# Optimization experiments

Measured on AMD Instinct MI355X. Metric: run time of the kernel, lower is better.

## Reference

```python
import jax, jax.numpy as jnp
import numpy as np

N, L, D, H, R = 16384, 8, 256, 256, 64  # nodes, chain len, input dim, hidden dim, rel dim


def setup_inputs() -> dict:
    key = jax.random.key(0)
    ks = jax.random.split(key, 10)
    s = 1.0 / np.sqrt(H)
    f32 = jnp.float32
    return {
        "left_chain": jax.random.normal(ks[0], (N, L, D), f32),
        "right_chain": jax.random.normal(ks[1], (N, L, D), f32),
        "rel": jax.random.normal(ks[2], (N, R), f32),
        "Wih_l": jax.random.normal(ks[3], (4 * H, D), f32) * s,
        "Whh_l": jax.random.normal(ks[4], (4 * H, H), f32) * s,
        "bih_l": jnp.zeros((4 * H,), f32),
        "bhh_l": jnp.zeros((4 * H,), f32),
        "Wih_r": jax.random.normal(ks[5], (4 * H, D), f32) * s,
        "Whh_r": jax.random.normal(ks[6], (4 * H, H), f32) * s,
        "bih_r": jnp.zeros((4 * H,), f32),
        "bhh_r": jnp.zeros((4 * H,), f32),
        "Wenc": jax.random.normal(ks[7], (H, 2 * H + R), f32) * s,
        "benc": jnp.zeros((H,), f32),
    }


def _lstm_last(x, Wih, Whh, bih, bhh):
    # x: [N, L, D]; PyTorch LSTM gate order i, f, g, o; zero initial state.
    n = x.shape[0]
    h0 = jnp.zeros((n, Whh.shape[1]), x.dtype)
    b = bih + bhh

    def step(carry, xt):
        h, c = carry
        g = xt @ Wih.T + h @ Whh.T + b  # [N, 4H]
        i, f, gg, o = jnp.split(g, 4, axis=-1)
        c = jax.nn.sigmoid(f) * c + jax.nn.sigmoid(i) * jnp.tanh(gg)
        h = jax.nn.sigmoid(o) * jnp.tanh(c)
        return (h, c), None

    (h, _c), _ = jax.lax.scan(step, (h0, h0), jnp.swapaxes(x, 0, 1))
    return h  # final hidden state [N, H]


def reference(left_chain, right_chain, rel,
              Wih_l, Whh_l, bih_l, bhh_l,
              Wih_r, Whh_r, bih_r, bhh_r,
              Wenc, benc):
    hl = _lstm_last(left_chain, Wih_l, Whh_l, bih_l, bhh_l)   # el(t)
    hr = _lstm_last(right_chain, Wih_r, Whh_r, bih_r, bhh_r)  # er(t)
    con = jnp.concatenate([hl, hr, rel], axis=-1)             # [N, 2H+R]
    return jnp.tanh(con @ Wenc.T + benc)                      # enc(t): [N, H]
```

## Files before the change

kernel.cpp:

```cpp
#include <hip/hip_runtime.h>
#include <hip/hip_fp16.h>

#define N_NODES 16384
#define SEQ_L   8
#define DIM_D   256
#define DIM_H   256
#define DIM_R   64

typedef float    f32x4 __attribute__((ext_vector_type(4)));
typedef _Float16 f16x8 __attribute__((ext_vector_type(8)));
typedef _Float16 f16x4 __attribute__((ext_vector_type(4)));

__device__ __forceinline__ float fsig(float x) {
    return __builtin_amdgcn_rcpf(1.f + __expf(-x));
}
__device__ __forceinline__ float ftanh(float x) {
    return 1.f - 2.f * __builtin_amdgcn_rcpf(1.f + __expf(2.f * x));
}

__global__ void prep_kernel(const float* __restrict__ Wih_l, const float* __restrict__ Whh_l,
                            const float* __restrict__ Wih_r, const float* __restrict__ Whh_r,
                            const float* __restrict__ Wenc,  const float* __restrict__ rel,
                            _Float16* __restrict__ pih_l, _Float16* __restrict__ phh_l,
                            _Float16* __restrict__ pih_r, _Float16* __restrict__ phh_r,
                            _Float16* __restrict__ penc,  _Float16* __restrict__ rel16) {
    const int stride = gridDim.x * blockDim.x;
    const int t0 = blockIdx.x * blockDim.x + threadIdx.x;

    const float* SW[4] = {Wih_l, Whh_l, Wih_r, Whh_r};
    _Float16*    DW[4] = {pih_l, phh_l, pih_r, phh_r};
    for (int m = 0; m < 4; ++m) {
        const float* W = SW[m];
        _Float16*    P = DW[m];
        for (int i8 = t0; i8 < 32768; i8 += stride) {
            int w    = i8 >> 12;
            int rem  = i8 & 4095;
            int f    = rem >> 6;
            int lane = rem & 63;
            int g    = f >> 4;
            int ht   = (f >> 3) & 1;
            int ks   = f & 7;
            int col  = g * 256 + w * 32 + ht * 16 + (lane & 15);
            int k    = ks * 32 + (lane >> 4) * 8;
            const float* s = W + (size_t)col * 256 + k;
            f32x4 v0 = *(const f32x4*)s;
            f32x4 v1 = *(const f32x4*)(s + 4);
            f16x8 h;
            h[0] = (_Float16)v0[0]; h[1] = (_Float16)v0[1];
            h[2] = (_Float16)v0[2]; h[3] = (_Float16)v0[3];
            h[4] = (_Float16)v1[0]; h[5] = (_Float16)v1[1];
            h[6] = (_Float16)v1[2]; h[7] = (_Float16)v1[3];
            *(f16x8*)&P[(size_t)i8 * 8] = h;
        }
    }

    for (int i8 = t0; i8 < 18432; i8 += stride) {
        int w    = i8 / 4608;
        int rem  = i8 - w * 4608;
        int f    = rem >> 6;
        int lane = rem & 63;
        int ct   = f / 18;
        int ks   = f - ct * 18;
        int col  = w * 64 + ct * 16 + (lane & 15);
        int k    = ks * 32 + (lane >> 4) * 8;
        const float* s = Wenc + (size_t)col * 576 + k;
        f32x4 v0 = *(const f32x4*)s;
        f32x4 v1 = *(const f32x4*)(s + 4);
        f16x8 h;
        h[0] = (_Float16)v0[0]; h[1] = (_Float16)v0[1];
        h[2] = (_Float16)v0[2]; h[3] = (_Float16)v0[3];
        h[4] = (_Float16)v1[0]; h[5] = (_Float16)v1[1];
        h[6] = (_Float16)v1[2]; h[7] = (_Float16)v1[3];
        *(f16x8*)&penc[(size_t)i8 * 8] = h;
    }

    const int nq = (N_NODES * DIM_R) / 8;
    for (int i = t0; i < nq; i += stride) {
        f32x4 v0 = *(const f32x4*)(rel + (size_t)i * 8);
        f32x4 v1 = *(const f32x4*)(rel + (size_t)i * 8 + 4);
        f16x8 h;
        h[0] = (_Float16)v0[0]; h[1] = (_Float16)v0[1];
        h[2] = (_Float16)v0[2]; h[3] = (_Float16)v0[3];
        h[4] = (_Float16)v1[0]; h[5] = (_Float16)v1[1];
        h[6] = (_Float16)v1[2]; h[7] = (_Float16)v1[3];
        *(f16x8*)&rel16[(size_t)i * 8] = h;
    }
}

__global__ __launch_bounds__(512, 2) void lstm_kernel(
    const float* __restrict__ left, const float* __restrict__ right,
    const _Float16* __restrict__ pih_l, const _Float16* __restrict__ phh_l,
    const _Float16* __restrict__ pih_r, const _Float16* __restrict__ phh_r,
    const float* __restrict__ bih_l, const float* __restrict__ bhh_l,
    const float* __restrict__ bih_r, const float* __restrict__ bhh_r,
    _Float16* __restrict__ hl_out, _Float16* __restrict__ hr_out) {

    const int side = blockIdx.y;
    const float*    chain = side ? right : left;
    const float*    bih   = side ? bih_r : bih_l;
    const float*    bhh   = side ? bhh_r : bhh_l;
    _Float16*       hout  = side ? hr_out : hl_out;

    __shared__ _Float16 lds[2 * 64 * 256] __attribute__((aligned(16)));

    const int tid  = threadIdx.x;
    const int lane = tid & 63;
    const int wave = tid >> 6;
    const int wu   = __builtin_amdgcn_readfirstlane(wave);
    const int l15  = lane & 15;
    const int l4   = lane >> 4;
    const int klb  = l4 * 8;
    const int node0 = blockIdx.x * 64;
    const int hid0  = wu * 32;

    const _Float16* Pih = (side ? pih_r : pih_l) + wu * 32768;
    const _Float16* Phh = (side ? phh_r : phh_l) + wu * 32768;

    const f32x4 FZ = {0.f, 0.f, 0.f, 0.f};

    float bias[4][2];
#pragma unroll
    for (int g = 0; g < 4; ++g)
#pragma unroll
        for (int ht = 0; ht < 2; ++ht) {
            int col = g * 256 + hid0 + ht * 16 + l15;
            bias[g][ht] = bih[col] + bhh[col];
        }

    f32x4 acc[4][4][2];
    f32x4 cst[4][2];
#pragma unroll
    for (int rt = 0; rt < 4; ++rt)
#pragma unroll
        for (int ht = 0; ht < 2; ++ht) cst[rt][ht] = FZ;

    int abase[4];
#pragma unroll
    for (int rt = 0; rt < 4; ++rt) {
        int row = rt * 16 + l15;
        abase[rt] = row * 256 + (klb ^ ((row & 3) << 3));
    }

    auto do_gemm = [&](const int lds_ofs, const _Float16* Pw) {
#pragma unroll
        for (int ks = 0; ks < 8; ++ks) {
            f16x8 a[4];
#pragma unroll
            for (int rt = 0; rt < 4; ++rt)
                a[rt] = *(const f16x8*)&lds[lds_ofs + abase[rt] + ks * 32];
            f16x8 b[8];
#pragma unroll
            for (int f = 0; f < 8; ++f)
                b[f] = *(const f16x8*)&Pw[(f * 8 + ks) * 512 + (lane << 3)];
#pragma unroll
            for (int g = 0; g < 4; ++g)
#pragma unroll
                for (int ht = 0; ht < 2; ++ht)
#pragma unroll
                    for (int rt = 0; rt < 4; ++rt)
                        acc[rt][g][ht] = __builtin_amdgcn_mfma_f32_16x16x32_f16(
                            a[rt], b[g * 2 + ht], acc[rt][g][ht], 0, 0, 0);
        }
    };

#pragma unroll 1
    for (int t = 0; t < SEQ_L; ++t) {
#pragma unroll
        for (int it = 0; it < 8; ++it) {
            int e4  = it * 512 + tid;
            int row = e4 >> 6;
            int kq  = (e4 & 63) << 2;
            f32x4 v = __builtin_nontemporal_load((const f32x4*)(chain +
                      (size_t)(node0 + row) * (SEQ_L * DIM_D) + t * DIM_D + kq));
            f16x4 h4;
            h4[0] = (_Float16)v[0]; h4[1] = (_Float16)v[1];
            h4[2] = (_Float16)v[2]; h4[3] = (_Float16)v[3];
            *(f16x4*)&lds[row * 256 + (kq ^ ((row & 3) << 3))] = h4;
        }
        __syncthreads();

#pragma unroll
        for (int rt = 0; rt < 4; ++rt)
#pragma unroll
            for (int g = 0; g < 4; ++g)
#pragma unroll
                for (int ht = 0; ht < 2; ++ht) acc[rt][g][ht] = FZ;

        do_gemm(0, Pih);
        if (t > 0) do_gemm(16384, Phh);
        __syncthreads();

#pragma unroll
        for (int rt = 0; rt < 4; ++rt)
#pragma unroll
            for (int ht = 0; ht < 2; ++ht)
#pragma unroll
                for (int r = 0; r < 4; ++r) {
                    float gi = acc[rt][0][ht][r] + bias[0][ht];
                    float gf = acc[rt][1][ht][r] + bias[1][ht];
                    float gg = acc[rt][2][ht][r] + bias[2][ht];
                    float go = acc[rt][3][ht][r] + bias[3][ht];
                    float ii = fsig(gi), ff = fsig(gf);
                    float gt = ftanh(gg), oo = fsig(go);
                    float c = ff * cst[rt][ht][r] + ii * gt;
                    cst[rt][ht][r] = c;
                    float h = oo * ftanh(c);
                    int rowl = rt * 16 + l4 * 4 + r;
                    int hid  = hid0 + ht * 16 + l15;
                    lds[16384 + rowl * 256 + (hid ^ ((rowl & 3) << 3))] = (_Float16)h;
                }
    }

    __syncthreads();
    {
        int row = tid >> 3;
        int seg = (tid & 7) * 32;
        _Float16* dst = hout + (size_t)(node0 + row) * 256 + seg;
        int sw = (row & 3) << 3;
#pragma unroll
        for (int j = 0; j < 4; ++j) {
            f16x8 v = *(const f16x8*)&lds[16384 + row * 256 + ((seg + j * 8) ^ sw)];
            __builtin_nontemporal_store(v, (f16x8*)(dst + j * 8));
        }
    }
}

__global__ __launch_bounds__(256, 2) void enc_kernel(
    const _Float16* __restrict__ hl, const _Float16* __restrict__ hr,
    const _Float16* __restrict__ rel16, const _Float16* __restrict__ penc,
    const float* __restrict__ benc, float* __restrict__ out) {

    const int tid  = threadIdx.x;
    const int lane = tid & 63;
    const int wave = tid >> 6;
    const int wu   = __builtin_amdgcn_readfirstlane(wave);
    const int l15  = lane & 15;
    const int l4   = lane >> 4;
    const int klb  = l4 * 8;
    const int row0 = blockIdx.x * 64;
    const int colw = wu * 64;

    const _Float16* Pw = penc + wu * 36864;

    const f32x4 FZ = {0.f, 0.f, 0.f, 0.f};
    f32x4 acc[4][4];
#pragma unroll
    for (int rt = 0; rt < 4; ++rt)
#pragma unroll
        for (int ct = 0; ct < 4; ++ct) acc[rt][ct] = FZ;

    float bce[4];
#pragma unroll
    for (int ct = 0; ct < 4; ++ct) bce[ct] = benc[colw + ct * 16 + l15];

    for (int ks = 0; ks < 18; ++ks) {
        const int kk = ks * 32 + klb;
        f16x8 a[4];
#pragma unroll
        for (int rt = 0; rt < 4; ++rt) {
            int row = row0 + rt * 16 + l15;
            const _Float16* p;
            if (ks < 8)       p = hl    + (size_t)row * 256 + kk;
            else if (ks < 16) p = hr    + (size_t)row * 256 + (kk - 256);
            else              p = rel16 + (size_t)row * 64  + (kk - 512);
            a[rt] = *(const f16x8*)p;
        }
#pragma unroll
        for (int ct = 0; ct < 4; ++ct) {
            f16x8 b = *(const f16x8*)&Pw[(ct * 18 + ks) * 512 + (lane << 3)];
#pragma unroll
            for (int rt = 0; rt < 4; ++rt)
                acc[rt][ct] = __builtin_amdgcn_mfma_f32_16x16x32_f16(
                    a[rt], b, acc[rt][ct], 0, 0, 0);
        }
    }

#pragma unroll
    for (int rt = 0; rt < 4; ++rt)
#pragma unroll
        for (int ct = 0; ct < 4; ++ct)
#pragma unroll
            for (int r = 0; r < 4; ++r) {
                int row = row0 + rt * 16 + l4 * 4 + r;
                int col = colw + ct * 16 + l15;
                out[(size_t)row * 256 + col] = ftanh(acc[rt][ct][r] + bce[ct]);
            }
}

extern "C" void kernel_launch(void* const* d_in, const int* in_sizes, int n_in,
                              void* d_out, int out_size, void* d_ws, size_t ws_size,
                              hipStream_t stream) {
    const float* left  = (const float*)d_in[0];
    const float* right = (const float*)d_in[1];
    const float* rel   = (const float*)d_in[2];
    const float* Wih_l = (const float*)d_in[3];
    const float* Whh_l = (const float*)d_in[4];
    const float* bih_l = (const float*)d_in[5];
    const float* bhh_l = (const float*)d_in[6];
    const float* Wih_r = (const float*)d_in[7];
    const float* Whh_r = (const float*)d_in[8];
    const float* bih_r = (const float*)d_in[9];
    const float* bhh_r = (const float*)d_in[10];
    const float* Wenc  = (const float*)d_in[11];
    const float* benc  = (const float*)d_in[12];
    float* out = (float*)d_out;

    char* ws = (char*)d_ws;
    _Float16* pih_l = (_Float16*)(ws);
    _Float16* phh_l = (_Float16*)(ws + 512 * 1024);
    _Float16* pih_r = (_Float16*)(ws + 1024 * 1024);
    _Float16* phh_r = (_Float16*)(ws + 1536 * 1024);
    _Float16* penc  = (_Float16*)(ws + 2048 * 1024);
    _Float16* rel16 = (_Float16*)(ws + 2560 * 1024);
    _Float16* hl16  = (_Float16*)(ws + 4608 * 1024);
    _Float16* hr16  = (_Float16*)(ws + 4608 * 1024 + 8192 * 1024);
    (void)in_sizes; (void)n_in; (void)out_size; (void)ws_size;

    hipLaunchKernelGGL(prep_kernel, dim3(512), dim3(256), 0, stream,
                       Wih_l, Whh_l, Wih_r, Whh_r, Wenc, rel,
                       pih_l, phh_l, pih_r, phh_r, penc, rel16);

    hipLaunchKernelGGL(lstm_kernel, dim3(N_NODES / 64, 2), dim3(512), 0, stream,
                       left, right, pih_l, phh_l, pih_r, phh_r,
                       bih_l, bhh_l, bih_r, bhh_r, hl16, hr16);

    hipLaunchKernelGGL(enc_kernel, dim3(N_NODES / 64), dim3(256), 0, stream,
                       hl16, hr16, rel16, penc, benc, out);
}
```

Before: 1.401 ms.

## Shrink LSTM tile to 32 nodes with 16 waves of 16 hidden units each

The LSTM kernel is retiled from 64 nodes × 8 waves (32 hidden units per wave) to 32 nodes × 16 waves (16 hidden units per wave). The weight prepacking layout changes to match. This cuts accumulator registers and LDS per block, which allows more blocks per CU and better latency hiding. In exchange, each weight fragment loaded from global/L2 is reused across only two row tiles instead of four, so weight traffic per node doubles.

```diff
diff --git a/kernel.cpp b/kernel.cpp
--- a/kernel.cpp
+++ b/kernel.cpp
@@ -33,14 +33,13 @@
         const float* W = SW[m];
         _Float16*    P = DW[m];
         for (int i8 = t0; i8 < 32768; i8 += stride) {
-            int w    = i8 >> 12;
-            int rem  = i8 & 4095;
+            int w    = i8 >> 11;
+            int rem  = i8 & 2047;
             int f    = rem >> 6;
             int lane = rem & 63;
-            int g    = f >> 4;
-            int ht   = (f >> 3) & 1;
-            int ks   = f & 7;
-            int col  = g * 256 + w * 32 + ht * 16 + (lane & 15);
+            int ks   = f >> 2;
+            int g    = f & 3;
+            int col  = g * 256 + w * 16 + (lane & 15);
             int k    = ks * 32 + (lane >> 4) * 8;
             const float* s = W + (size_t)col * 256 + k;
             f32x4 v0 = *(const f32x4*)s;
@@ -87,7 +86,7 @@
     }
 }
 
-__global__ __launch_bounds__(512, 2) void lstm_kernel(
+__global__ __launch_bounds__(1024, 4) void lstm_kernel(
     const float* __restrict__ left, const float* __restrict__ right,
     const _Float16* __restrict__ pih_l, const _Float16* __restrict__ phh_l,
     const _Float16* __restrict__ pih_r, const _Float16* __restrict__ phh_r,
@@ -101,7 +100,8 @@
     const float*    bhh   = side ? bhh_r : bhh_l;
     _Float16*       hout  = side ? hr_out : hl_out;
 
-    __shared__ _Float16 lds[2 * 64 * 256] __attribute__((aligned(16)));
+    __shared__ _Float16 lds[2 * 32 * 256] __attribute__((aligned(16)));
+    const int HOFF = 32 * 256;
 
     const int tid  = threadIdx.x;
     const int lane = tid & 63;
@@ -110,33 +110,28 @@
     const int l15  = lane & 15;
     const int l4   = lane >> 4;
     const int klb  = l4 * 8;
-    const int node0 = blockIdx.x * 64;
-    const int hid0  = wu * 32;
-
-    const _Float16* Pih = (side ? pih_r : pih_l) + wu * 32768;
-    const _Float16* Phh = (side ? phh_r : phh_l) + wu * 32768;
+    const int node0 = blockIdx.x * 32;
+    const int hid0  = wu * 16;
+
+    const _Float16* Pih = (side ? pih_r : pih_l) + wu * 16384;
+    const _Float16* Phh = (side ? phh_r : phh_l) + wu * 16384;
 
     const f32x4 FZ = {0.f, 0.f, 0.f, 0.f};
 
-    float bias[4][2];
-#pragma unroll
-    for (int g = 0; g < 4; ++g)
-#pragma unroll
-        for (int ht = 0; ht < 2; ++ht) {
-            int col = g * 256 + hid0 + ht * 16 + l15;
-            bias[g][ht] = bih[col] + bhh[col];
-        }
-
-    f32x4 acc[4][4][2];
-    f32x4 cst[4][2];
-#pragma unroll
-    for (int rt = 0; rt < 4; ++rt)
-#pragma unroll
-        for (int ht = 0; ht < 2; ++ht) cst[rt][ht] = FZ;
-
-    int abase[4];
-#pragma unroll
-    for (int rt = 0; rt < 4; ++rt) {
+    float bias[4];
+#pragma unroll
+    for (int g = 0; g < 4; ++g) {
+        int col = g * 256 + hid0 + l15;
+        bias[g] = bih[col] + bhh[col];
+    }
+
+    f32x4 acc[2][4];
+    f32x4 cst[2];
+    cst[0] = FZ; cst[1] = FZ;
+
+    int abase[2];
+#pragma unroll
+    for (int rt = 0; rt < 2; ++rt) {
         int row = rt * 16 + l15;
         abase[rt] = row * 256 + (klb ^ ((row & 3) << 3));
     }
@@ -144,30 +139,28 @@
     auto do_gemm = [&](const int lds_ofs, const _Float16* Pw) {
 #pragma unroll
         for (int ks = 0; ks < 8; ++ks) {
-            f16x8 a[4];
-#pragma unroll
-            for (int rt = 0; rt < 4; ++rt)
+            f16x8 a[2];
+#pragma unroll
+            for (int rt = 0; rt < 2; ++rt)
                 a[rt] = *(const f16x8*)&lds[lds_ofs + abase[rt] + ks * 32];
-            f16x8 b[8];
-#pragma unroll
-            for (int f = 0; f < 8; ++f)
-                b[f] = *(const f16x8*)&Pw[(f * 8 + ks) * 512 + (lane << 3)];
+            f16x8 b[4];
 #pragma unroll
             for (int g = 0; g < 4; ++g)
-#pragma unroll
-                for (int ht = 0; ht < 2; ++ht)
-#pragma unroll
-                    for (int rt = 0; rt < 4; ++rt)
-                        acc[rt][g][ht] = __builtin_amdgcn_mfma_f32_16x16x32_f16(
-                            a[rt], b[g * 2 + ht], acc[rt][g][ht], 0, 0, 0);
+                b[g] = *(const f16x8*)&Pw[(ks * 4 + g) * 512 + (lane << 3)];
+#pragma unroll
+            for (int g = 0; g < 4; ++g)
+#pragma unroll
+                for (int rt = 0; rt < 2; ++rt)
+                    acc[rt][g] = __builtin_amdgcn_mfma_f32_16x16x32_f16(
+                        a[rt], b[g], acc[rt][g], 0, 0, 0);
         }
     };
 
 #pragma unroll 1
     for (int t = 0; t < SEQ_L; ++t) {
 #pragma unroll
-        for (int it = 0; it < 8; ++it) {
-            int e4  = it * 512 + tid;
+        for (int it = 0; it < 2; ++it) {
+            int e4  = it * 1024 + tid;
             int row = e4 >> 6;
             int kq  = (e4 & 63) << 2;
             f32x4 v = __builtin_nontemporal_load((const f32x4*)(chain +
@@ -180,48 +173,39 @@
         __syncthreads();
 
 #pragma unroll
-        for (int rt = 0; rt < 4; ++rt)
-#pragma unroll
-            for (int g = 0; g < 4; ++g)
-#pragma unroll
-                for (int ht = 0; ht < 2; ++ht) acc[rt][g][ht] = FZ;
+        for (int rt = 0; rt < 2; ++rt)
+#pragma unroll
+            for (int g = 0; g < 4; ++g) acc[rt][g] = FZ;
 
         do_gemm(0, Pih);
-        if (t > 0) do_gemm(16384, Phh);
+        if (t > 0) do_gemm(HOFF, Phh);
         __syncthreads();
 
 #pragma unroll
-        for (int rt = 0; rt < 4; ++rt)
-#pragma unroll
-            for (int ht = 0; ht < 2; ++ht)
-#pragma unroll
-                for (int r = 0; r < 4; ++r) {
-                    float gi = acc[rt][0][ht][r] + bias[0][ht];
-                    float gf = acc[rt][1][ht][r] + bias[1][ht];
-                    float gg = acc[rt][2][ht][r] + bias[2][ht];
-                    float go = acc[rt][3][ht][r] + bias[3][ht];
-                    float ii = fsig(gi), ff = fsig(gf);
-                    float gt = ftanh(gg), oo = fsig(go);
-                    float c = ff * cst[rt][ht][r] + ii * gt;
-                    cst[rt][ht][r] = c;
-                    float h = oo * ftanh(c);
-                    int rowl = rt * 16 + l4 * 4 + r;
-                    int hid  = hid0 + ht * 16 + l15;
-                    lds[16384 + rowl * 256 + (hid ^ ((rowl & 3) << 3))] = (_Float16)h;
-                }
+        for (int rt = 0; rt < 2; ++rt)
+#pragma unroll
+            for (int r = 0; r < 4; ++r) {
+                float gi = acc[rt][0][r] + bias[0];
+                float gf = acc[rt][1][r] + bias[1];
+                float gg = acc[rt][2][r] + bias[2];
+                float go = acc[rt][3][r] + bias[3];
+                float ii = fsig(gi), ff = fsig(gf);
+                float gt = ftanh(gg), oo = fsig(go);
+                float c = ff * cst[rt][r] + ii * gt;
+                cst[rt][r] = c;
+                float h = oo * ftanh(c);
+                int rowl = rt * 16 + l4 * 4 + r;
+                int hid  = hid0 + l15;
+                lds[HOFF + rowl * 256 + (hid ^ ((rowl & 3) << 3))] = (_Float16)h;
+            }
     }
 
     __syncthreads();
     {
-        int row = tid >> 3;
-        int seg = (tid & 7) * 32;
-        _Float16* dst = hout + (size_t)(node0 + row) * 256 + seg;
-        int sw = (row & 3) << 3;
-#pragma unroll
-        for (int j = 0; j < 4; ++j) {
-            f16x8 v = *(const f16x8*)&lds[16384 + row * 256 + ((seg + j * 8) ^ sw)];
-            __builtin_nontemporal_store(v, (f16x8*)(dst + j * 8));
-        }
+        int row = tid >> 5;
+        int seg = (tid & 31) * 8;
+        f16x8 v = *(const f16x8*)&lds[HOFF + row * 256 + (seg ^ ((row & 3) << 3))];
+        __builtin_nontemporal_store(v, (f16x8*)(hout + (size_t)(node0 + row) * 256 + seg));
     }
 }
 
@@ -320,7 +304,7 @@
                        Wih_l, Whh_l, Wih_r, Whh_r, Wenc, rel,
                        pih_l, phh_l, pih_r, phh_r, penc, rel16);
 
-    hipLaunchKernelGGL(lstm_kernel, dim3(N_NODES / 64, 2), dim3(512), 0, stream,
+    hipLaunchKernelGGL(lstm_kernel, dim3(N_NODES / 32, 2), dim3(1024), 0, stream,
                        left, right, pih_l, phh_l, pih_r, phh_r,
                        bih_l, bhh_l, bih_r, bhh_r, hl16, hr16);
 
```

Measured after the change: 1.302 ms. 7.0% less time.
